# Performance work log

Hardware: AMD Instinct MI355X
Metric: run time of the kernel (lower is better)

## Reference

```python
import jax, jax.numpy as jnp
import numpy as np

HID = 1024
H = 8
HD = HID // H  # 128; KV length must equal HD for the bias-add broadcast
B = 8
LQ = 4096
LK = HD


def setup_inputs() -> dict:
    key = jax.random.key(0)
    ks = jax.random.split(key, 16)
    s = 0.02
    inp = {
        "query": jax.random.normal(ks[0], (B, LQ, HID), jnp.float32),
        "key": jax.random.normal(ks[1], (B, LK, HID), jnp.float32),
        "value": jax.random.normal(ks[2], (B, LK, HID), jnp.float32),
        "atten": jax.random.normal(ks[3], (B, LQ, HID), jnp.float32),
        "mask": jax.random.randint(ks[4], (B, 1, 1, LK), 0, 2, jnp.int32),
        "Wq": jax.random.normal(ks[5], (HID, HID), jnp.float32) * s,
        "bq": jnp.zeros((HID,), jnp.float32),
        "Wk": jax.random.normal(ks[6], (HID, HID), jnp.float32) * s,
        "bk": jnp.zeros((HID,), jnp.float32),
        "Wv": jax.random.normal(ks[7], (HID, HID), jnp.float32) * s,
        "bv": jnp.zeros((HID,), jnp.float32),
        "Watt": jax.random.normal(ks[8], (HID, HID), jnp.float32) * s,
        "batt": jnp.zeros((HID,), jnp.float32),
        "Wfc": jax.random.normal(ks[9], (HID, HID), jnp.float32) * s,
        "bfc": jnp.zeros((HID,), jnp.float32),
    }
    return inp


def _heads(x):
    # [B, L, HID] -> [B, H, L, HD]
    b, l, _ = x.shape
    return x.reshape(b, l, H, HD).transpose(0, 2, 1, 3)


def reference(query, key, value, atten, mask, Wq, bq, Wk, bk, Wv, bv, Watt, batt, Wfc, bfc):
    scale = jnp.sqrt(jnp.asarray(HD, jnp.float32))
    atten_out = _heads(atten @ Watt.T + batt)          # [B,H,LQ,HD]
    Q = _heads(query @ Wq.T + bq)                      # [B,H,LQ,HD]
    K = _heads(key @ Wk.T + bk)                        # [B,H,LK,HD]
    V = _heads(value @ Wv.T + bv)                      # [B,H,LK,HD]
    energy = jnp.einsum('bhqd,bhkd->bhqk', Q, K) / scale + atten_out  # LK == HD
    energy = jnp.where(mask == 0, jnp.float32(-1e10), energy)
    attention = jax.nn.softmax(energy, axis=-1)
    x = jnp.einsum('bhqk,bhkd->bhqd', attention, V)
    x = x.transpose(0, 2, 1, 3).reshape(query.shape[0], -1, HID)
    return x @ Wfc.T + bfc
```

## Files before the change

### kernel.cpp

```cpp
#include <hip/hip_runtime.h>
#include <hip/hip_bf16.h>
#include <stdint.h>

typedef __bf16 bf16_t;
typedef __bf16 bf16x8 __attribute__((ext_vector_type(8)));
typedef float f32x4 __attribute__((ext_vector_type(4)));

#define HIDN 1024
#define NHEAD 8
#define HDIM 128
#define NBATCH 8
#define LQLEN 4096
#define LKLEN 128

__device__ __forceinline__ void gload_lds16(const void* g, void* l) {
  __builtin_amdgcn_global_load_lds(
      (const __attribute__((address_space(1))) unsigned int*)g,
      (__attribute__((address_space(3))) unsigned int*)l, 16, 0, 0);
}

__global__ __launch_bounds__(256) void convk7(
    const float* s0, const float* s1, const float* s2, const float* s3,
    const float* s4, const float* s5, const float* s6,
    bf16_t* d0, bf16_t* d1, bf16_t* d2, bf16_t* d3,
    bf16_t* d4, bf16_t* d5, bf16_t* d6) {
  const float* src; bf16_t* dst;
  switch (blockIdx.y) {
    case 0: src = s0; dst = d0; break;
    case 1: src = s1; dst = d1; break;
    case 2: src = s2; dst = d2; break;
    case 3: src = s3; dst = d3; break;
    case 4: src = s4; dst = d4; break;
    case 5: src = s5; dst = d5; break;
    default: src = s6; dst = d6; break;
  }
  const int n4 = (1024 * 1024) / 4;
  const int stride = gridDim.x * 256;
  for (int i = blockIdx.x * 256 + threadIdx.x; i < n4; i += stride) {
    const float4 v = ((const float4*)src)[i];
    bf16x8 o;
    o[0] = (bf16_t)v.x; o[1] = (bf16_t)v.y; o[2] = (bf16_t)v.z; o[3] = (bf16_t)v.w;
    *(uint2*)((char*)dst + (size_t)i * 8) = *(uint2*)&o;
  }
}

template <int MODE, bool AF32>
__device__ __forceinline__ void gemm8p_body(const void* __restrict__ Asrc,
                                            const bf16_t* __restrict__ Bw,
                                            const float* __restrict__ bias,
                                            void* __restrict__ Cout,
                                            char* smem, int bid) {
  constexpr int NT = 32;
  constexpr int SLOT = 32768;

  const int tid = threadIdx.x;
  const int wid = tid >> 6, lane = tid & 63;
  const int lr = lane & 15, lh = lane >> 4;
  const int wr = wid >> 2, wc = wid & 3;

  const int m_blk = (bid & 7) * 16 + (bid >> 5);
  const int n_blk = (bid >> 3) & 3;
  const int m0 = m_blk * 256, n0 = n_blk * 256;

  const int c0 = tid, c1 = tid + 512;
  const int sl0 = ((c0 & 3) ^ ((c0 >> 3) & 3));
  const int sl1 = ((c1 & 3) ^ ((c1 >> 3) & 3));
  const char* srcB0 = (const char*)Bw + (size_t)(n0 + (c0 >> 2)) * 2048 + (sl0 << 4);
  const char* srcB1 = (const char*)Bw + (size_t)(n0 + (c1 >> 2)) * 2048 + (sl1 << 4);
  const int dA0 = c0 * 16, dA1 = c1 * 16;
  const int dB0 = 16384 + c0 * 16, dB1 = 16384 + c1 * 16;

  f32x4 acc[8][4] = {};

  const int swz = ((lr >> 1) & 3) << 4;
  const int aoff = (wr * 128 + lr) * 64 + ((lh << 4) ^ swz);
  const int boff = 16384 + (wc * 64 + lr) * 64 + ((lh << 4) ^ swz);

#define GLOADB(T)                                                     \
  do {                                                                \
    char* bdst = smem + (((T) & 3) * SLOT) + 16384;                   \
    gload_lds16(srcB0 + (T) * 64, bdst + dA0);                        \
    gload_lds16(srcB1 + (T) * 64, bdst + dA1);                        \
  } while (0)

  if constexpr (AF32) {
    const char* srcAf0 = (const char*)Asrc + (size_t)(m0 + (c0 >> 2)) * 4096 + sl0 * 32;
    const char* srcAf1 = (const char*)Asrc + (size_t)(m0 + (c1 >> 2)) * 4096 + sl1 * 32;

    f32x4 eA0, eA1, eA2, eA3, oA0, oA1, oA2, oA3;

#define ISSUE_A(R0, R1, R2, R3, T)                                    \
  do {                                                                \
    R0 = *(const f32x4*)(srcAf0 + (T) * 128);                         \
    R1 = *(const f32x4*)(srcAf0 + (T) * 128 + 16);                    \
    R2 = *(const f32x4*)(srcAf1 + (T) * 128);                         \
    R3 = *(const f32x4*)(srcAf1 + (T) * 128 + 16);                    \
  } while (0)

#define WRITE_A(SL, R0, R1, R2, R3)                                   \
  do {                                                                \
    bf16x8 w0, w1;                                                    \
    w0[0] = (bf16_t)R0[0]; w0[1] = (bf16_t)R0[1];                     \
    w0[2] = (bf16_t)R0[2]; w0[3] = (bf16_t)R0[3];                     \
    w0[4] = (bf16_t)R1[0]; w0[5] = (bf16_t)R1[1];                     \
    w0[6] = (bf16_t)R1[2]; w0[7] = (bf16_t)R1[3];                     \
    w1[0] = (bf16_t)R2[0]; w1[1] = (bf16_t)R2[1];                     \
    w1[2] = (bf16_t)R2[2]; w1[3] = (bf16_t)R2[3];                     \
    w1[4] = (bf16_t)R3[0]; w1[5] = (bf16_t)R3[1];                     \
    w1[6] = (bf16_t)R3[2]; w1[7] = (bf16_t)R3[3];                     \
    *(bf16x8*)(smem + (SL) * SLOT + dA0) = w0;                        \
    *(bf16x8*)(smem + (SL) * SLOT + dA1) = w1;                        \
  } while (0)

    GLOADB(0); GLOADB(1); GLOADB(2);
    ISSUE_A(eA0, eA1, eA2, eA3, 0);
    ISSUE_A(oA0, oA1, oA2, oA3, 1);
    asm volatile("" ::: "memory");
    asm volatile("s_waitcnt vmcnt(0)" ::: "memory");
    WRITE_A(0, eA0, eA1, eA2, eA3);
    WRITE_A(1, oA0, oA1, oA2, oA3);
    ISSUE_A(eA0, eA1, eA2, eA3, 2);
    ISSUE_A(oA0, oA1, oA2, oA3, 3);
    asm volatile("" ::: "memory");
    asm volatile("s_waitcnt vmcnt(8) lgkmcnt(0)" ::: "memory");
    __builtin_amdgcn_s_barrier();
    __builtin_amdgcn_sched_barrier(0);

#define GTILE(T, R0, R1, R2, R3)                                          \
  do {                                                                    \
    const char* sA = smem + ((T) & 3) * SLOT + aoff;                      \
    const char* sB = smem + ((T) & 3) * SLOT + boff;                      \
    if ((T) <= NT - 3) WRITE_A(((T) + 2) & 3, R0, R1, R2, R3);            \
    if ((T) <= NT - 4) GLOADB((T) + 3);                                   \
    if ((T) <= NT - 5) ISSUE_A(R0, R1, R2, R3, (T) + 4);                  \
    bf16x8 bfr[4], af[8];                                                 \
    _Pragma("unroll") for (int n = 0; n < 4; ++n)                         \
        bfr[n] = *(const bf16x8*)(sB + n * 1024);                         \
    _Pragma("unroll") for (int m = 0; m < 8; ++m)                         \
        af[m] = *(const bf16x8*)(sA + m * 1024);                          \
    __builtin_amdgcn_s_setprio(1);                                        \
    _Pragma("unroll") for (int m = 0; m < 8; ++m)                         \
        _Pragma("unroll") for (int n = 0; n < 4; ++n)                     \
            acc[m][n] = __builtin_amdgcn_mfma_f32_16x16x32_bf16(          \
                af[m], bfr[n], acc[m][n], 0, 0, 0);                       \
    __builtin_amdgcn_s_setprio(0);                                        \
    if ((T) < NT - 1) {                                                   \
      __builtin_amdgcn_sched_barrier(0);                                  \
      if ((T) <= NT - 5)                                                  \
        asm volatile("s_waitcnt vmcnt(10) lgkmcnt(0)" ::: "memory");      \
      else if ((T) == NT - 4)                                             \
        asm volatile("s_waitcnt vmcnt(2) lgkmcnt(0)" ::: "memory");       \
      else                                                                \
        asm volatile("s_waitcnt vmcnt(0) lgkmcnt(0)" ::: "memory");       \
      __builtin_amdgcn_s_barrier();                                       \
      __builtin_amdgcn_sched_barrier(0);                                  \
    }                                                                     \
  } while (0)

    for (int tt = 0; tt < NT / 2; ++tt) {
      GTILE(2 * tt, eA0, eA1, eA2, eA3);
      GTILE(2 * tt + 1, oA0, oA1, oA2, oA3);
    }
#undef GTILE
#undef ISSUE_A
#undef WRITE_A
  } else {
    const char* srcA0 = (const char*)Asrc + (size_t)(m0 + (c0 >> 2)) * 2048 + (sl0 << 4);
    const char* srcA1 = (const char*)Asrc + (size_t)(m0 + (c1 >> 2)) * 2048 + (sl1 << 4);
#pragma unroll
    for (int tt = 0; tt < 3; ++tt) {
      char* dst = smem + tt * SLOT;
      gload_lds16(srcA0 + tt * 64, dst + dA0);
      gload_lds16(srcA1 + tt * 64, dst + dA1);
      gload_lds16(srcB0 + tt * 64, dst + dB0);
      gload_lds16(srcB1 + tt * 64, dst + dB1);
    }
    asm volatile("s_waitcnt vmcnt(8)" ::: "memory");
    __builtin_amdgcn_s_barrier();
    __builtin_amdgcn_sched_barrier(0);

    for (int t = 0; t < NT; ++t) {
      const char* sA = smem + (t & 3) * SLOT + aoff;
      const char* sB = smem + (t & 3) * SLOT + boff;
      char* dst = smem + ((t + 3) & 3) * SLOT;
      const int kb = (t + 3) * 64;
      const bool pf = (t <= NT - 4);

      bf16x8 bfr[4], af[8];
#pragma unroll
      for (int n = 0; n < 4; ++n) bfr[n] = *(const bf16x8*)(sB + n * 1024);
#pragma unroll
      for (int m = 0; m < 8; ++m) af[m] = *(const bf16x8*)(sA + m * 1024);
      if (pf) {
        gload_lds16(srcA0 + kb, dst + dA0);
        gload_lds16(srcA1 + kb, dst + dA1);
        gload_lds16(srcB0 + kb, dst + dB0);
        gload_lds16(srcB1 + kb, dst + dB1);
      }
      __builtin_amdgcn_s_setprio(1);
#pragma unroll
      for (int m = 0; m < 8; ++m)
#pragma unroll
        for (int n = 0; n < 4; ++n)
          acc[m][n] = __builtin_amdgcn_mfma_f32_16x16x32_bf16(af[m], bfr[n], acc[m][n], 0, 0, 0);
      __builtin_amdgcn_s_setprio(0);

      if (t < NT - 1) {
        __builtin_amdgcn_sched_barrier(0);
        if (t <= NT - 4)
          asm volatile("s_waitcnt vmcnt(8)" ::: "memory");
        else if (t == NT - 3)
          asm volatile("s_waitcnt vmcnt(4)" ::: "memory");
        else
          asm volatile("s_waitcnt vmcnt(0)" ::: "memory");
        __builtin_amdgcn_s_barrier();
        __builtin_amdgcn_sched_barrier(0);
      }
    }
  }
#undef GLOADB

  if constexpr (MODE == 2) {
    float* C = (float*)Cout;
#pragma unroll
    for (int f = 0; f < 8; ++f) {
      const int gm = m0 + wr * 128 + f * 16 + lh * 4;
#pragma unroll
      for (int j = 0; j < 4; ++j) {
        const int gn = n0 + wc * 64 + j * 16 + lr;
        const float bb = bias[gn];
#pragma unroll
        for (int r = 0; r < 4; ++r)
          C[(size_t)(gm + r) * HIDN + gn] = acc[f][j][r] + bb;
      }
    }
  } else {
    __builtin_amdgcn_s_barrier();
    __builtin_amdgcn_sched_barrier(0);
    char* wlds = smem + wid * 16384;
#pragma unroll
    for (int f = 0; f < 8; ++f) {
#pragma unroll
      for (int j = 0; j < 4; ++j) {
        const int gn = n0 + wc * 64 + j * 16 + lr;
        const float bb = bias[gn];
#pragma unroll
        for (int r = 0; r < 4; ++r) {
          const int row = f * 16 + lh * 4 + r;
          const int col2 = ((j * 16 + lr) * 2) ^ ((row & 7) << 4);
          *(bf16_t*)(wlds + row * 128 + col2) = (bf16_t)(acc[f][j][r] + bb);
        }
      }
    }
    asm volatile("s_waitcnt lgkmcnt(0)" ::: "memory");
    __builtin_amdgcn_sched_barrier(0);
    bf16_t* C = (bf16_t*)Cout;
    const int gnb = n0 + wc * 64;
    const int h = gnb >> 7, dd = gnb & 127;
#pragma unroll
    for (int p = 0; p < 16; ++p) {
      const int rl = p * 8 + (lane >> 3);
      const int cb = ((lane & 7) * 16) ^ ((rl & 7) << 4);
      const uint4 v = *(const uint4*)(wlds + rl * 128 + cb);
      const int gm = m0 + wr * 128 + rl;
      const int b = gm >> 12, l = gm & 4095;
      char* dstp = (char*)(C + (((size_t)(b * NHEAD + h) * LQLEN + l) << 7) + dd) +
                   (((lane & 7) * 16));
      *(uint4*)dstp = v;
    }
  }
}

__global__ __launch_bounds__(512, 2) void gemm_qa(
    const float* __restrict__ Aq, const bf16_t* __restrict__ Wq,
    const float* __restrict__ bq, bf16_t* __restrict__ Qh,
    const float* __restrict__ Aa, const bf16_t* __restrict__ Wa,
    const float* __restrict__ ba, bf16_t* __restrict__ Ah) {
  __shared__ uint4 smem_raw[8192];
  const int bid = blockIdx.x;
  if (bid < 512)
    gemm8p_body<0, true>(Aq, Wq, bq, (void*)Qh, (char*)smem_raw, bid);
  else
    gemm8p_body<0, true>(Aa, Wa, ba, (void*)Ah, (char*)smem_raw, bid - 512);
}

__global__ __launch_bounds__(512, 2) void gemm_fc(const bf16_t* __restrict__ A,
                                                  const bf16_t* __restrict__ Bw,
                                                  const float* __restrict__ bias,
                                                  float* __restrict__ Cout) {
  __shared__ uint4 smem_raw[8192];
  gemm8p_body<2, false>(A, Bw, bias, (void*)Cout, (char*)smem_raw, blockIdx.x);
}

__global__ __launch_bounds__(256) void gemm_btkv(
    const bf16_t* __restrict__ kA, const bf16_t* __restrict__ kW,
    const float* __restrict__ kb_, bf16_t* __restrict__ Kh,
    const bf16_t* __restrict__ vA, const bf16_t* __restrict__ vW,
    const float* __restrict__ vb_, bf16_t* __restrict__ Vt) {
  constexpr int BK = 32;
  __shared__ uint4 AsRaw[128 * BK * 2 / 16];
  __shared__ uint4 BsRaw[128 * BK * 2 / 16];
  bf16_t* As = (bf16_t*)AsRaw;
  bf16_t* Bs = (bf16_t*)BsRaw;

  const bool isV = (blockIdx.z == 1);
  const bf16_t* A = isV ? vA : kA;
  const bf16_t* Bw = isV ? vW : kW;
  const float* bias = isV ? vb_ : kb_;
  bf16_t* Cout = isV ? Vt : Kh;

  const int tid = threadIdx.x;
  const int wid = tid >> 6;
  const int lane = tid & 63;
  const int lr = lane & 15, lh = lane >> 4;
  const int m0 = blockIdx.x * 128, n0 = blockIdx.y * 128;
  const int wm = (wid >> 1) * 64, wn = (wid & 1) * 64;

  f32x4 acc[4][4] = {};

  const int srow = lane >> 2;
  const int scol = (lane & 3) * 16;

  for (int k0 = 0; k0 < HIDN; k0 += BK) {
#pragma unroll
    for (int i = 0; i < 2; ++i) {
      const int c = wid + i * 4;
      const int row = c * 16 + srow;
      gload_lds16((const char*)A + ((size_t)(m0 + row) * HIDN + k0) * 2 + scol,
                  (char*)As + c * 1024);
      gload_lds16((const char*)Bw + ((size_t)(n0 + row) * HIDN + k0) * 2 + scol,
                  (char*)Bs + c * 1024);
    }
    __syncthreads();

    bf16x8 af[4], bfr[4];
#pragma unroll
    for (int i = 0; i < 4; ++i) {
      af[i]  = *(const bf16x8*)(As + (wm + i * 16 + lr) * BK + lh * 8);
      bfr[i] = *(const bf16x8*)(Bs + (wn + i * 16 + lr) * BK + lh * 8);
    }
#pragma unroll
    for (int i = 0; i < 4; ++i)
#pragma unroll
      for (int j = 0; j < 4; ++j)
        acc[i][j] = __builtin_amdgcn_mfma_f32_16x16x32_bf16(af[i], bfr[j], acc[i][j], 0, 0, 0);
    __syncthreads();
  }

#pragma unroll
  for (int i = 0; i < 4; ++i) {
#pragma unroll
    for (int r = 0; r < 4; ++r) {
      const int gm = m0 + wm + i * 16 + lh * 4 + r;
#pragma unroll
      for (int j = 0; j < 4; ++j) {
        const int gn = n0 + wn + j * 16 + lr;
        const float v = acc[i][j][r] + bias[gn];
        const int b = gm >> 7, l = gm & 127;
        const int h = gn >> 7, d = gn & 127;
        size_t idx;
        if (!isV)
          idx = (((size_t)(b * NHEAD + h) * 128 + l) << 7) + d;
        else
          idx = (((size_t)(b * NHEAD + h) * 128 + d) << 7) + l;
        Cout[idx] = (bf16_t)v;
      }
    }
  }
}

__global__ __launch_bounds__(256) void attn_kernel(
    const bf16_t* __restrict__ Qh, const bf16_t* __restrict__ Ah,
    const bf16_t* __restrict__ Kh, const bf16_t* __restrict__ Vt,
    const int* __restrict__ mask, bf16_t* __restrict__ X) {
  __shared__ uint4 KsRaw[2048];
  __shared__ uint4 VsRaw[2048];
  __shared__ float Ms[128];
  char* Ks = (char*)KsRaw;
  char* Vs = (char*)VsRaw;

  const int tid = threadIdx.x, wid = tid >> 6, lane = tid & 63;
  const int lr = lane & 15, lh = lane >> 4;

  const int lin = blockIdx.y * 64 + blockIdx.x;
  const int nid = (lin & 7) * 512 + (lin >> 3);
  const int bh = nid >> 6, b = bh >> 3, h = bh & 7;
  const int q0 = (nid & 63) * 64;

  {
    const char* Kg = (const char*)(Kh + (size_t)bh * 16384);
    const char* Vg = (const char*)(Vt + (size_t)bh * 16384);
#pragma unroll
    for (int it = 0; it < 8; ++it) {
      const int e = it * 256 + tid;
      const int row = e >> 4;
      const int cbp = (e & 15) << 4;
      const int srcoff = row * 256 + (cbp ^ ((row & 7) << 4));
      gload_lds16(Kg + srcoff, Ks + e * 16);
      gload_lds16(Vg + srcoff, Vs + e * 16);
    }
  }
  if (tid < 128) Ms[tid] = (mask[b * 128 + tid] == 0) ? 0.f : 1.f;

  bf16x8 qf[4];
  {
    const bf16_t* Qb = Qh + ((size_t)bh * LQLEN + q0 + wid * 16 + lr) * 128;
#pragma unroll
    for (int s = 0; s < 4; ++s) qf[s] = *(const bf16x8*)(Qb + s * 32 + lh * 8);
  }
  asm volatile("s_waitcnt vmcnt(0)" ::: "memory");
  __syncthreads();

  f32x4 acc[8] = {};
#pragma unroll
  for (int nt = 0; nt < 8; ++nt) {
#pragma unroll
    for (int s = 0; s < 4; ++s) {
      const int row = nt * 16 + lr;
      const int cb = (s * 64 + lh * 16) ^ ((row & 7) << 4);
      const bf16x8 kf = *(const bf16x8*)(Ks + row * 256 + cb);
      acc[nt] = __builtin_amdgcn_mfma_f32_16x16x32_bf16(qf[s], kf, acc[nt], 0, 0, 0);
    }
  }
  __syncthreads();

  {
    const char* Ag = (const char*)(Ah + ((size_t)bh * LQLEN + q0) * 128);
#pragma unroll
    for (int it = 0; it < 4; ++it) {
      const int c = it * 256 + tid;
      gload_lds16(Ag + c * 16, Ks + 16384 + c * 16);
    }
  }
  asm volatile("s_waitcnt vmcnt(0)" ::: "memory");
  __syncthreads();
  const char* Al = Ks + 16384;

  float ex[8][4];
  float rsum[4];
  const float sc = 0.08838834764831845f;
#pragma unroll
  for (int r = 0; r < 4; ++r) {
    const int row = lh * 4 + r;
    const int rowg = wid * 16 + row;
    float mx = -3.0e38f;
#pragma unroll
    for (int nt = 0; nt < 8; ++nt) {
      const int col = nt * 16 + lr;
      float e = acc[nt][r] * sc + (float)(*(const bf16_t*)(Al + rowg * 256 + col * 2));
      e = (Ms[col] != 0.f) ? e : -1.0e10f;
      ex[nt][r] = e;
      mx = fmaxf(mx, e);
    }
    mx = fmaxf(mx, __shfl_xor(mx, 1));
    mx = fmaxf(mx, __shfl_xor(mx, 2));
    mx = fmaxf(mx, __shfl_xor(mx, 4));
    mx = fmaxf(mx, __shfl_xor(mx, 8));
    float s_ = 0.f;
#pragma unroll
    for (int nt = 0; nt < 8; ++nt) {
      const float p = __expf(ex[nt][r] - mx);
      ex[nt][r] = p;
      s_ += p;
    }
    s_ += __shfl_xor(s_, 1);
    s_ += __shfl_xor(s_, 2);
    s_ += __shfl_xor(s_, 4);
    s_ += __shfl_xor(s_, 8);
    rsum[r] = s_;
  }

  char* Pb = Ks + wid * 4096;
#pragma unroll
  for (int r = 0; r < 4; ++r) {
    const int row = lh * 4 + r;
#pragma unroll
    for (int nt = 0; nt < 8; ++nt) {
      const int col = nt * 16 + lr;
      const int off = (row * 256 + col * 2) ^ ((row & 7) << 4);
      *(bf16_t*)(Pb + off) = (bf16_t)ex[nt][r];
    }
  }
  __syncthreads();

  bf16x8 pf[4];
#pragma unroll
  for (int s = 0; s < 4; ++s)
    pf[s] = *(const bf16x8*)(Pb + lr * 256 + ((s * 64 + lh * 16) ^ ((lr & 7) << 4)));
  f32x4 acc2[8] = {};
#pragma unroll
  for (int nt = 0; nt < 8; ++nt) {
#pragma unroll
    for (int s = 0; s < 4; ++s) {
      const int row = nt * 16 + lr;
      const int cb = (s * 64 + lh * 16) ^ ((row & 7) << 4);
      const bf16x8 vf = *(const bf16x8*)(Vs + row * 256 + cb);
      acc2[nt] = __builtin_amdgcn_mfma_f32_16x16x32_bf16(pf[s], vf, acc2[nt], 0, 0, 0);
    }
  }
  __syncthreads();

  float rs[4];
#pragma unroll
  for (int r = 0; r < 4; ++r) rs[r] = 1.f / rsum[r];
#pragma unroll
  for (int nt = 0; nt < 8; ++nt)
#pragma unroll
    for (int r = 0; r < 4; ++r)
      *(bf16_t*)(Vs + (wid * 16 + lh * 4 + r) * 256 + (nt * 16 + lr) * 2) =
          (bf16_t)(acc2[nt][r] * rs[r]);
  asm volatile("s_waitcnt lgkmcnt(0)" ::: "memory");
  __syncthreads();

#pragma unroll
  for (int it = 0; it < 4; ++it) {
    const int c = it * 256 + tid;
    const int row = c >> 4;
    const int off = (c & 15) << 4;
    const uint4 v = *(const uint4*)(Vs + row * 256 + off);
    char* dstp = (char*)(X + ((size_t)(b * LQLEN) + q0 + row) * HIDN + h * 128) + off;
    *(uint4*)dstp = v;
  }
}

extern "C" void kernel_launch(void* const* d_in, const int* in_sizes, int n_in,
                              void* d_out, int out_size, void* d_ws, size_t ws_size,
                              hipStream_t stream) {
  const float* query = (const float*)d_in[0];
  const float* key   = (const float*)d_in[1];
  const float* value = (const float*)d_in[2];
  const float* atten = (const float*)d_in[3];
  const int*   mask  = (const int*)d_in[4];
  const float* Wq  = (const float*)d_in[5];  const float* bq   = (const float*)d_in[6];
  const float* Wk  = (const float*)d_in[7];  const float* bk   = (const float*)d_in[8];
  const float* Wv  = (const float*)d_in[9];  const float* bv   = (const float*)d_in[10];
  const float* Wat = (const float*)d_in[11]; const float* batt = (const float*)d_in[12];
  const float* Wfc = (const float*)d_in[13]; const float* bfc  = (const float*)d_in[14];

  char* ws = (char*)d_ws;
  bf16_t* X   = (bf16_t*)(ws + 0x0000000);
  bf16_t* Qh  = (bf16_t*)(ws + 0x8000000);
  bf16_t* Ah  = (bf16_t*)(ws + 0xC000000);
  char* sm = ws + 0x10000000;
  bf16_t* kbf = (bf16_t*)(sm + 0x000000);
  bf16_t* vbf = (bf16_t*)(sm + 0x200000);
  bf16_t* wqb = (bf16_t*)(sm + 0x400000);
  bf16_t* wkb = (bf16_t*)(sm + 0x600000);
  bf16_t* wvb = (bf16_t*)(sm + 0x800000);
  bf16_t* wab = (bf16_t*)(sm + 0xA00000);
  bf16_t* wfb = (bf16_t*)(sm + 0xC00000);
  bf16_t* Kh  = (bf16_t*)(sm + 0xE00000);
  bf16_t* Vt  = (bf16_t*)(sm + 0x1000000);

  convk7<<<dim3(256, 7), dim3(256), 0, stream>>>(
      key, value, Wq, Wk, Wv, Wat, Wfc,
      kbf, vbf, wqb, wkb, wvb, wab, wfb);

  gemm_btkv<<<dim3(8, 8, 2), dim3(256), 0, stream>>>(
      kbf, wkb, bk, Kh, vbf, wvb, bv, Vt);

  gemm_qa<<<dim3(1024), dim3(512), 0, stream>>>(
      query, wqb, bq, Qh, atten, wab, batt, Ah);

  attn_kernel<<<dim3(LQLEN / 64, NBATCH * NHEAD), dim3(256), 0, stream>>>(
      Qh, Ah, Kh, Vt, mask, X);

  gemm_fc<<<dim3(512), dim3(512), 0, stream>>>(X, wfb, bfc, (float*)d_out);
}
```

Before: 376.9 us.

## Process four query tiles per attention block to reuse staged K/V

Each attention block now loops over four 64-row query tiles, so the K and V tiles loaded into LDS are reused four times instead of being reloaded by four separate blocks. A dedicated LDS buffer holds the attention-bias tile and the per-wave P/output staging. Most block-wide barriers are replaced with per-wave waitcnt and scheduling barriers. The grid shrinks by four, which lowers parallelism and occupancy, and the extra LDS buffer raises per-block shared memory use.

```diff
diff --git a/kernel.cpp b/kernel.cpp
--- a/kernel.cpp
+++ b/kernel.cpp
@@ -375,17 +375,19 @@
     const int* __restrict__ mask, bf16_t* __restrict__ X) {
   __shared__ uint4 KsRaw[2048];
   __shared__ uint4 VsRaw[2048];
+  __shared__ uint4 ApRaw[1024];
   __shared__ float Ms[128];
   char* Ks = (char*)KsRaw;
   char* Vs = (char*)VsRaw;
+  char* Ap = (char*)ApRaw;
 
   const int tid = threadIdx.x, wid = tid >> 6, lane = tid & 63;
   const int lr = lane & 15, lh = lane >> 4;
 
-  const int lin = blockIdx.y * 64 + blockIdx.x;
-  const int nid = (lin & 7) * 512 + (lin >> 3);
-  const int bh = nid >> 6, b = bh >> 3, h = bh & 7;
-  const int q0 = (nid & 63) * 64;
+  const int lin = blockIdx.y * 16 + blockIdx.x;
+  const int nid = (lin & 7) * 128 + (lin >> 3);
+  const int bh = nid >> 4, b = bh >> 3, h = bh & 7;
+  const int q0b = (nid & 15) * 256;
 
   {
     const char* Kg = (const char*)(Kh + (size_t)bh * 16384);
@@ -401,125 +403,131 @@
     }
   }
   if (tid < 128) Ms[tid] = (mask[b * 128 + tid] == 0) ? 0.f : 1.f;
-
-  bf16x8 qf[4];
-  {
-    const bf16_t* Qb = Qh + ((size_t)bh * LQLEN + q0 + wid * 16 + lr) * 128;
-#pragma unroll
-    for (int s = 0; s < 4; ++s) qf[s] = *(const bf16x8*)(Qb + s * 32 + lh * 8);
-  }
   asm volatile("s_waitcnt vmcnt(0)" ::: "memory");
   __syncthreads();
 
-  f32x4 acc[8] = {};
-#pragma unroll
-  for (int nt = 0; nt < 8; ++nt) {
-#pragma unroll
-    for (int s = 0; s < 4; ++s) {
-      const int row = nt * 16 + lr;
-      const int cb = (s * 64 + lh * 16) ^ ((row & 7) << 4);
-      const bf16x8 kf = *(const bf16x8*)(Ks + row * 256 + cb);
-      acc[nt] = __builtin_amdgcn_mfma_f32_16x16x32_bf16(qf[s], kf, acc[nt], 0, 0, 0);
-    }
-  }
-  __syncthreads();
-
-  {
-    const char* Ag = (const char*)(Ah + ((size_t)bh * LQLEN + q0) * 128);
+  const float sc = 0.08838834764831845f;
+  char* Pb = Ap + wid * 4096;
+
+  for (int qs = 0; qs < 4; ++qs) {
+    const int q0 = q0b + qs * 64;
+
+    if (qs) __syncthreads();
+
+    {
+      const char* Ag = (const char*)(Ah + ((size_t)bh * LQLEN + q0) * 128);
+#pragma unroll
+      for (int it = 0; it < 4; ++it) {
+        const int c = it * 256 + tid;
+        gload_lds16(Ag + c * 16, Ap + c * 16);
+      }
+    }
+    bf16x8 qf[4];
+    {
+      const bf16_t* Qb = Qh + ((size_t)bh * LQLEN + q0 + wid * 16 + lr) * 128;
+#pragma unroll
+      for (int s = 0; s < 4; ++s) qf[s] = *(const bf16x8*)(Qb + s * 32 + lh * 8);
+    }
+    asm volatile("s_waitcnt vmcnt(0)" ::: "memory");
+    __syncthreads();
+
+    f32x4 acc[8] = {};
+#pragma unroll
+    for (int nt = 0; nt < 8; ++nt) {
+#pragma unroll
+      for (int s = 0; s < 4; ++s) {
+        const int row = nt * 16 + lr;
+        const int cb = (s * 64 + lh * 16) ^ ((row & 7) << 4);
+        const bf16x8 kf = *(const bf16x8*)(Ks + row * 256 + cb);
+        acc[nt] = __builtin_amdgcn_mfma_f32_16x16x32_bf16(qf[s], kf, acc[nt], 0, 0, 0);
+      }
+    }
+
+    float ex[8][4];
+    float rsum[4];
+#pragma unroll
+    for (int r = 0; r < 4; ++r) {
+      const int row = lh * 4 + r;
+      const int rowg = wid * 16 + row;
+      float mx = -3.0e38f;
+#pragma unroll
+      for (int nt = 0; nt < 8; ++nt) {
+        const int col = nt * 16 + lr;
+        float e = acc[nt][r] * sc + (float)(*(const bf16_t*)(Ap + rowg * 256 + col * 2));
+        e = (Ms[col] != 0.f) ? e : -1.0e10f;
+        ex[nt][r] = e;
+        mx = fmaxf(mx, e);
+      }
+      mx = fmaxf(mx, __shfl_xor(mx, 1));
+      mx = fmaxf(mx, __shfl_xor(mx, 2));
+      mx = fmaxf(mx, __shfl_xor(mx, 4));
+      mx = fmaxf(mx, __shfl_xor(mx, 8));
+      float s_ = 0.f;
+#pragma unroll
+      for (int nt = 0; nt < 8; ++nt) {
+        const float p = __expf(ex[nt][r] - mx);
+        ex[nt][r] = p;
+        s_ += p;
+      }
+      s_ += __shfl_xor(s_, 1);
+      s_ += __shfl_xor(s_, 2);
+      s_ += __shfl_xor(s_, 4);
+      s_ += __shfl_xor(s_, 8);
+      rsum[r] = s_;
+    }
+
+#pragma unroll
+    for (int r = 0; r < 4; ++r) {
+      const int row = lh * 4 + r;
+#pragma unroll
+      for (int nt = 0; nt < 8; ++nt) {
+        const int col = nt * 16 + lr;
+        const int off = (row * 256 + col * 2) ^ ((row & 7) << 4);
+        *(bf16_t*)(Pb + off) = (bf16_t)ex[nt][r];
+      }
+    }
+    asm volatile("s_waitcnt lgkmcnt(0)" ::: "memory");
+    __builtin_amdgcn_sched_barrier(0);
+
+    bf16x8 pf[4];
+#pragma unroll
+    for (int s = 0; s < 4; ++s)
+      pf[s] = *(const bf16x8*)(Pb + lr * 256 + ((s * 64 + lh * 16) ^ ((lr & 7) << 4)));
+    f32x4 acc2[8] = {};
+#pragma unroll
+    for (int nt = 0; nt < 8; ++nt) {
+#pragma unroll
+      for (int s = 0; s < 4; ++s) {
+        const int row = nt * 16 + lr;
+        const int cb = (s * 64 + lh * 16) ^ ((row & 7) << 4);
+        const bf16x8 vf = *(const bf16x8*)(Vs + row * 256 + cb);
+        acc2[nt] = __builtin_amdgcn_mfma_f32_16x16x32_bf16(pf[s], vf, acc2[nt], 0, 0, 0);
+      }
+    }
+
+    asm volatile("s_waitcnt lgkmcnt(0)" ::: "memory");
+    __builtin_amdgcn_sched_barrier(0);
+    float rs[4];
+#pragma unroll
+    for (int r = 0; r < 4; ++r) rs[r] = 1.f / rsum[r];
+#pragma unroll
+    for (int nt = 0; nt < 8; ++nt)
+#pragma unroll
+      for (int r = 0; r < 4; ++r)
+        *(bf16_t*)(Pb + (lh * 4 + r) * 256 + (nt * 16 + lr) * 2) =
+            (bf16_t)(acc2[nt][r] * rs[r]);
+    asm volatile("s_waitcnt lgkmcnt(0)" ::: "memory");
+    __builtin_amdgcn_sched_barrier(0);
 #pragma unroll
     for (int it = 0; it < 4; ++it) {
-      const int c = it * 256 + tid;
-      gload_lds16(Ag + c * 16, Ks + 16384 + c * 16);
-    }
-  }
-  asm volatile("s_waitcnt vmcnt(0)" ::: "memory");
-  __syncthreads();
-  const char* Al = Ks + 16384;
-
-  float ex[8][4];
-  float rsum[4];
-  const float sc = 0.08838834764831845f;
-#pragma unroll
-  for (int r = 0; r < 4; ++r) {
-    const int row = lh * 4 + r;
-    const int rowg = wid * 16 + row;
-    float mx = -3.0e38f;
-#pragma unroll
-    for (int nt = 0; nt < 8; ++nt) {
-      const int col = nt * 16 + lr;
-      float e = acc[nt][r] * sc + (float)(*(const bf16_t*)(Al + rowg * 256 + col * 2));
-      e = (Ms[col] != 0.f) ? e : -1.0e10f;
-      ex[nt][r] = e;
-      mx = fmaxf(mx, e);
-    }
-    mx = fmaxf(mx, __shfl_xor(mx, 1));
-    mx = fmaxf(mx, __shfl_xor(mx, 2));
-    mx = fmaxf(mx, __shfl_xor(mx, 4));
-    mx = fmaxf(mx, __shfl_xor(mx, 8));
-    float s_ = 0.f;
-#pragma unroll
-    for (int nt = 0; nt < 8; ++nt) {
-      const float p = __expf(ex[nt][r] - mx);
-      ex[nt][r] = p;
-      s_ += p;
-    }
-    s_ += __shfl_xor(s_, 1);
-    s_ += __shfl_xor(s_, 2);
-    s_ += __shfl_xor(s_, 4);
-    s_ += __shfl_xor(s_, 8);
-    rsum[r] = s_;
-  }
-
-  char* Pb = Ks + wid * 4096;
-#pragma unroll
-  for (int r = 0; r < 4; ++r) {
-    const int row = lh * 4 + r;
-#pragma unroll
-    for (int nt = 0; nt < 8; ++nt) {
-      const int col = nt * 16 + lr;
-      const int off = (row * 256 + col * 2) ^ ((row & 7) << 4);
-      *(bf16_t*)(Pb + off) = (bf16_t)ex[nt][r];
-    }
-  }
-  __syncthreads();
-
-  bf16x8 pf[4];
-#pragma unroll
-  for (int s = 0; s < 4; ++s)
-    pf[s] = *(const bf16x8*)(Pb + lr * 256 + ((s * 64 + lh * 16) ^ ((lr & 7) << 4)));
-  f32x4 acc2[8] = {};
-#pragma unroll
-  for (int nt = 0; nt < 8; ++nt) {
-#pragma unroll
-    for (int s = 0; s < 4; ++s) {
-      const int row = nt * 16 + lr;
-      const int cb = (s * 64 + lh * 16) ^ ((row & 7) << 4);
-      const bf16x8 vf = *(const bf16x8*)(Vs + row * 256 + cb);
-      acc2[nt] = __builtin_amdgcn_mfma_f32_16x16x32_bf16(pf[s], vf, acc2[nt], 0, 0, 0);
-    }
-  }
-  __syncthreads();
-
-  float rs[4];
-#pragma unroll
-  for (int r = 0; r < 4; ++r) rs[r] = 1.f / rsum[r];
-#pragma unroll
-  for (int nt = 0; nt < 8; ++nt)
-#pragma unroll
-    for (int r = 0; r < 4; ++r)
-      *(bf16_t*)(Vs + (wid * 16 + lh * 4 + r) * 256 + (nt * 16 + lr) * 2) =
-          (bf16_t)(acc2[nt][r] * rs[r]);
-  asm volatile("s_waitcnt lgkmcnt(0)" ::: "memory");
-  __syncthreads();
-
-#pragma unroll
-  for (int it = 0; it < 4; ++it) {
-    const int c = it * 256 + tid;
-    const int row = c >> 4;
-    const int off = (c & 15) << 4;
-    const uint4 v = *(const uint4*)(Vs + row * 256 + off);
-    char* dstp = (char*)(X + ((size_t)(b * LQLEN) + q0 + row) * HIDN + h * 128) + off;
-    *(uint4*)dstp = v;
+      const int c = it * 64 + lane;
+      const int row = c >> 4;
+      const int off = (c & 15) << 4;
+      const uint4 v = *(const uint4*)(Pb + row * 256 + off);
+      char* dstp = (char*)(X + ((size_t)(b * LQLEN) + q0 + wid * 16 + row) * HIDN +
+                           h * 128) + off;
+      *(uint4*)dstp = v;
+    }
   }
 }
 
@@ -562,7 +570,7 @@
   gemm_qa<<<dim3(1024), dim3(512), 0, stream>>>(
       query, wqb, bq, Qh, atten, wab, batt, Ah);
 
-  attn_kernel<<<dim3(LQLEN / 64, NBATCH * NHEAD), dim3(256), 0, stream>>>(
+  attn_kernel<<<dim3(16, 64), dim3(256), 0, stream>>>(
       Qh, Ah, Kh, Vt, mask, X);
 
   gemm_fc<<<dim3(512), dim3(512), 0, stream>>>(X, wfb, bfc, (float*)d_out);
```

Result: slower. 396.7 us (+5.3%).
